# Kernel optimization log

Hardware: AMD Instinct MI355X
Metric: run time of the kernel (lower is better)

Reference implementation:

```python
import jax, jax.numpy as jnp
import numpy as np

N = 50000
V = 3
DIM = 128
H = 64


def setup_inputs() -> dict:
    key = jax.random.key(0)
    ks = jax.random.split(key, 8)
    x = jax.random.normal(ks[0], (N, V * DIM), dtype=jnp.float32)
    edge_index = jax.random.randint(ks[1], (2, 800000), 0, N, dtype=jnp.int64)
    Wv = jax.random.normal(ks[2], (V, DIM, H), dtype=jnp.float32) * (1.0 / np.sqrt(DIM))
    bv = jnp.zeros((V, H), dtype=jnp.float32)
    na_w = jax.random.normal(ks[3], (H, 1), dtype=jnp.float32) * (1.0 / np.sqrt(H))
    na_b = jnp.zeros((1,), dtype=jnp.float32)
    va_w1 = jax.random.normal(ks[4], (H, H // 2), dtype=jnp.float32) * (1.0 / np.sqrt(H))
    va_b1 = jnp.zeros((H // 2,), dtype=jnp.float32)
    va_w2 = jax.random.normal(ks[5], (H // 2, 1), dtype=jnp.float32) * (1.0 / np.sqrt(H // 2))
    va_b2 = jnp.zeros((1,), dtype=jnp.float32)
    cls_w = jax.random.normal(ks[6], (H, 2), dtype=jnp.float32) * (1.0 / np.sqrt(H))
    cls_b = jnp.zeros((2,), dtype=jnp.float32)
    return dict(x=x, edge_index=edge_index, Wv=Wv, bv=bv, na_w=na_w, na_b=na_b,
                va_w1=va_w1, va_b1=va_b1, va_w2=va_w2, va_b2=va_b2,
                cls_w=cls_w, cls_b=cls_b)


def reference(x, edge_index, Wv, bv, na_w, na_b, va_w1, va_b1, va_w2, va_b2, cls_w, cls_b):
    n = x.shape[0]
    # split into equal-dim views: [N, V, DIM]
    xv = x.reshape(n, V, DIM)

    # --- GCNConv (PyG defaults): linear transform, add self-loops, sym-norm aggregate, bias ---
    h = jnp.einsum('nvd,vdh->nvh', xv, Wv)  # [N, V, H]

    src = edge_index[0]
    dst = edge_index[1]
    loop = jnp.arange(n, dtype=src.dtype)
    src_full = jnp.concatenate([src, loop])
    dst_full = jnp.concatenate([dst, loop])

    ones = jnp.ones(src_full.shape[0], dtype=h.dtype)
    deg = jax.ops.segment_sum(ones, dst_full, num_segments=n)  # in-degree incl. self-loop
    dinv = jnp.where(deg > 0, 1.0 / jnp.sqrt(deg), 0.0)
    norm = dinv[src_full] * dinv[dst_full]  # [E+N]

    msgs = h[src_full] * norm[:, None, None]            # [E+N, V, H]
    agg = jax.ops.segment_sum(msgs, dst_full, num_segments=n)  # [N, V, H]
    agg = agg + bv[None, :, :]

    # ReLU
    emb = jax.nn.relu(agg)  # [N, V, H]

    # --- NodeAttentionLayer: softmax over nodes (dim=0), applied per view ---
    scores = jnp.einsum('nvh,ho->nvo', emb, na_w) + na_b  # [N, V, 1]
    att = jax.nn.softmax(scores, axis=0)
    emb_w = emb * att  # [N, V, H]

    # --- ViewAttention ---
    avg = jnp.mean(emb_w, axis=0)  # [V, H]
    vs = jnp.tanh(avg @ va_w1 + va_b1) @ va_w2 + va_b2  # [V, 1]
    vw = jax.nn.softmax(vs.T, axis=1)  # [1, V]
    fused = jnp.einsum('nvh,v->nh', emb_w, vw[0])  # [N, H]

    # --- classifier + log_softmax ---
    logits = fused @ cls_w + cls_b
    logp = jax.nn.log_softmax(logits, axis=1)
    return logp, fused, vw[0]
```

## Files before the change

kernel.cpp:

```cpp
#include <hip/hip_runtime.h>
#include <math.h>

#define NV 3
#define DIMX 128
#define HD 64
#define NVH 192
#define NBLK 256
#define NBUK 128
#define BSH 9

typedef unsigned int uint32;
typedef unsigned short ushort16;
typedef unsigned char uchar;
typedef __attribute__((ext_vector_type(8))) short short8;
typedef __attribute__((ext_vector_type(4))) float f32x4;

__device__ __forceinline__ unsigned fkey(float f){
  unsigned b = __float_as_uint(f);
  return (b & 0x80000000u) ? ~b : (b | 0x80000000u);
}
__device__ __forceinline__ float unkey(unsigned k){
  return __uint_as_float((k & 0x80000000u) ? (k ^ 0x80000000u) : ~k);
}
__device__ __forceinline__ uint32 bf16rne(float f){
  uint32 u = __float_as_uint(f);
  return (u + 0x7fffu + ((u >> 16) & 1u)) >> 16;
}
__device__ __forceinline__ float bfus(uint32 q){ return __uint_as_float(q << 16); }
__device__ __forceinline__ float ub0(uint32 p){ return (float)(p & 0xffu); }
__device__ __forceinline__ float ub1(uint32 p){ return (float)((p >> 8) & 0xffu); }
__device__ __forceinline__ float ub2(uint32 p){ return (float)((p >> 16) & 0xffu); }

__global__ void k_zero(float* __restrict__ wsum, float* __restrict__ sumexp, unsigned* __restrict__ maxkey){
  int t = threadIdx.x;
  if (t < NVH) wsum[t] = 0.f;
  else if (t < NVH+3) sumexp[t-NVH] = 0.f;
  else if (t < NVH+6) maxkey[t-NVH-3] = 0u;
}

__global__ __launch_bounds__(256) void k_hist(const int* __restrict__ ei, int E, int EPB,
                                              int* __restrict__ histT){
  __shared__ int sh[NBUK];
  int t = threadIdx.x, b = blockIdx.x;
  if (t < NBUK) sh[t] = 0;
  __syncthreads();
  int e0 = b*EPB, e1 = min(e0 + EPB, E);
  for (int i = e0 + t; i < e1; i += 256){
    int d = ei[E + i];
    atomicAdd(&sh[d >> BSH], 1);
  }
  __syncthreads();
  if (t < NBUK) histT[t*NBLK + b] = sh[t];
}

__global__ __launch_bounds__(1024) void k_hscan(int* __restrict__ histT){
  __shared__ int sh[1024];
  int t = threadIdx.x;
  int lo = t*32;
  int vals[32]; int s = 0;
  #pragma unroll
  for (int k = 0; k < 32; ++k){ vals[k] = histT[lo+k]; s += vals[k]; }
  sh[t] = s; __syncthreads();
  for (int ofs = 1; ofs < 1024; ofs <<= 1){
    int v = (t >= ofs) ? sh[t-ofs] : 0;
    __syncthreads();
    sh[t] += v;
    __syncthreads();
  }
  int run = sh[t] - s;
  #pragma unroll
  for (int k = 0; k < 32; ++k){ histT[lo+k] = run; run += vals[k]; }
}

__global__ __launch_bounds__(256) void k_scatter(const int* __restrict__ ei, int E, int EPB,
                                                 const int* __restrict__ ofsT, uint32* __restrict__ ebuf){
  __shared__ int cur[NBUK];
  int t = threadIdx.x, b = blockIdx.x;
  if (t < NBUK) cur[t] = ofsT[t*NBLK + b];
  __syncthreads();
  int e0 = b*EPB, e1 = min(e0 + EPB, E);
  for (int i = e0 + t; i < e1; i += 256){
    int s = ei[i], d = ei[E + i];
    int pos = atomicAdd(&cur[d >> BSH], 1);
    ebuf[pos] = ((uint32)(d & 511) << 16) | (uint32)s;
  }
}

__global__ __launch_bounds__(512) void k_csr(const uint32* __restrict__ ebuf, const int* __restrict__ ofsT,
                                             int E, int N, int* __restrict__ rowstart,
                                             float* __restrict__ dinv, int* __restrict__ csr){
  __shared__ int cnt[512];
  __shared__ int pre[512];
  int t = threadIdx.x, b = blockIdx.x;
  int estart = ofsT[b*NBLK];
  int eend   = ((b+1)*NBLK < NBUK*NBLK) ? ofsT[(b+1)*NBLK] : E;
  int n0 = b << BSH;
  int nn = min(512, N - n0);
  cnt[t] = 0;
  __syncthreads();
  for (int i = estart + t; i < eend; i += 512){
    atomicAdd(&cnt[ebuf[i] >> 16], 1);
  }
  __syncthreads();
  int c = cnt[t];
  pre[t] = c;
  __syncthreads();
  for (int ofs = 1; ofs < 512; ofs <<= 1){
    int v = (t >= ofs) ? pre[t-ofs] : 0;
    __syncthreads();
    pre[t] += v;
    __syncthreads();
  }
  int excl = pre[t] - c;
  if (t < nn){
    rowstart[n0 + t] = estart + excl;
    dinv[n0 + t] = rsqrtf((float)(c + 1));
  }
  if (b == gridDim.x - 1 && t == 0) rowstart[N] = E;
  cnt[t] = estart + excl;
  __syncthreads();
  for (int i = estart + t; i < eend; i += 512){
    uint32 e = ebuf[i];
    int pos = atomicAdd(&cnt[e >> 16], 1);
    csr[pos] = (int)(e & 0xFFFFu);
  }
}

__global__ __launch_bounds__(256) void k_wpack(const float* __restrict__ Wv, uint32* __restrict__ Wb){
  int t = blockIdx.x*blockDim.x + threadIdx.x;
  if (t >= 3072) return;
  int l = t & 63, s = (t >> 6) & 3, c = (t >> 8) & 3, v = t >> 10;
  int h = c*16 + (l & 15);
  int kbase = s*32 + (l >> 4)*8;
  const float* wp = Wv + v*8192 + h;
  uint32 o[4];
  #pragma unroll
  for (int jj = 0; jj < 4; ++jj){
    uint32 lo = bf16rne(wp[(kbase + 2*jj    )*64]);
    uint32 hi = bf16rne(wp[(kbase + 2*jj + 1)*64]);
    o[jj] = lo | (hi << 16);
  }
  Wb[t*4+0] = o[0]; Wb[t*4+1] = o[1]; Wb[t*4+2] = o[2]; Wb[t*4+3] = o[3];
}

__global__ __launch_bounds__(256) void k_h(const float* __restrict__ x, const uint32* __restrict__ Wb,
                                           const float* __restrict__ dinv,
                                           uchar* __restrict__ hq8, float* __restrict__ scale4,
                                           int N, int NT){
  int wv = (blockIdx.x*blockDim.x + threadIdx.x) >> 6;
  int lane = threadIdx.x & 63;
  int tile = wv / 3;
  int v = wv - tile*3;
  if (tile >= NT) return;
  int jrow = lane & 15;
  int kq   = lane >> 4;
  int nrow = tile*16 + jrow;
  const float* xr = x + (size_t)nrow*384 + v*128 + kq*8;
  const short8* WB = (const short8*)Wb;

  f32x4 acc[4] = {};
  #pragma unroll
  for (int s = 0; s < 4; ++s){
    const float* p = xr + s*32;
    float4 f = *(const float4*)p, g = *(const float4*)(p+4);
    short8 a;
    a[0]=(short)bf16rne(f.x); a[1]=(short)bf16rne(f.y); a[2]=(short)bf16rne(f.z); a[3]=(short)bf16rne(f.w);
    a[4]=(short)bf16rne(g.x); a[5]=(short)bf16rne(g.y); a[6]=(short)bf16rne(g.z); a[7]=(short)bf16rne(g.w);
    #pragma unroll
    for (int c = 0; c < 4; ++c){
      short8 b = WB[(v*4 + c)*256 + s*64 + lane];
      acc[c] = __builtin_amdgcn_mfma_f32_16x16x32_bf16(a, b, acc[c], 0, 0, 0);
    }
  }

  float vv[4][4];
  float mx = 0.f;
  #pragma unroll
  for (int r = 0; r < 4; ++r){
    int n = tile*16 + kq*4 + r;
    float dv = dinv[n];
    #pragma unroll
    for (int c = 0; c < 4; ++c){
      float t = acc[c][r]*dv;
      vv[c][r] = t;
      mx = fmaxf(mx, fabsf(t));
    }
  }
  #pragma unroll
  for (int ofs = 1; ofs < 64; ofs <<= 1) mx = fmaxf(mx, __shfl_xor(mx, ofs));
  float inv = (mx > 0.f) ? 127.0f/mx : 0.f;
  #pragma unroll
  for (int r = 0; r < 4; ++r){
    int n = tile*16 + kq*4 + r;
    #pragma unroll
    for (int c = 0; c < 4; ++c){
      uint32 q = (uint32)(int)(vv[c][r]*inv + 128.5f);
      hq8[(size_t)n*256 + (c*16 + jrow)*4 + v] = (uchar)q;
    }
  }
  if (lane == 0) scale4[tile*4 + v] = mx * (1.0f/127.0f);
}

__global__ __launch_bounds__(256) void k_aggv(const uint32* __restrict__ hq4, const float4* __restrict__ sc4,
                                              const int* __restrict__ rowstart, const int* __restrict__ csr,
                                              const float* __restrict__ dinv, const float* __restrict__ bv,
                                              const float* __restrict__ na_w, const float* __restrict__ na_b,
                                              ushort16* __restrict__ emb, float* __restrict__ scores, int N){
  int wid = (blockIdx.x*blockDim.x + threadIdx.x) >> 6;
  int lane = threadIdx.x & 63;
  if (wid >= N) return;
  int n = wid;
  uint32 ps = hq4[(size_t)n*64 + lane];
  float4 cs = sc4[n >> 4];
  float a0 = cs.x*ub0(ps), a1 = cs.y*ub1(ps), a2 = cs.z*ub2(ps);
  float ss0 = cs.x, ss1 = cs.y, ss2 = cs.z;
  int r0 = rowstart[n], r1 = rowstart[n+1];
  for (int base = r0; base < r1; base += 64){
    int m = r1 - base; if (m > 64) m = 64;
    int sv = (lane < m) ? __builtin_nontemporal_load(&csr[base + lane]) : 0;
    int i = 0;
    for (; i + 3 < m; i += 4){
      int s0 = __shfl(sv, i), s1 = __shfl(sv, i+1), s2 = __shfl(sv, i+2), s3 = __shfl(sv, i+3);
      uint32 p0 = hq4[(size_t)s0*64 + lane];
      uint32 p1 = hq4[(size_t)s1*64 + lane];
      uint32 p2 = hq4[(size_t)s2*64 + lane];
      uint32 p3 = hq4[(size_t)s3*64 + lane];
      float4 f0 = sc4[s0 >> 4];
      float4 f1 = sc4[s1 >> 4];
      float4 f2 = sc4[s2 >> 4];
      float4 f3 = sc4[s3 >> 4];
      a0 = fmaf(f0.x, ub0(p0), a0); a1 = fmaf(f0.y, ub1(p0), a1); a2 = fmaf(f0.z, ub2(p0), a2);
      a0 = fmaf(f1.x, ub0(p1), a0); a1 = fmaf(f1.y, ub1(p1), a1); a2 = fmaf(f1.z, ub2(p1), a2);
      a0 = fmaf(f2.x, ub0(p2), a0); a1 = fmaf(f2.y, ub1(p2), a1); a2 = fmaf(f2.z, ub2(p2), a2);
      a0 = fmaf(f3.x, ub0(p3), a0); a1 = fmaf(f3.y, ub1(p3), a1); a2 = fmaf(f3.z, ub2(p3), a2);
      ss0 += f0.x + f1.x + f2.x + f3.x;
      ss1 += f0.y + f1.y + f2.y + f3.y;
      ss2 += f0.z + f1.z + f2.z + f3.z;
    }
    for (; i < m; ++i){
      int s = __shfl(sv, i);
      uint32 p = hq4[(size_t)s*64 + lane];
      float4 f = sc4[s >> 4];
      a0 = fmaf(f.x, ub0(p), a0); a1 = fmaf(f.y, ub1(p), a1); a2 = fmaf(f.z, ub2(p), a2);
      ss0 += f.x; ss1 += f.y; ss2 += f.z;
    }
  }
  a0 -= 128.0f*ss0;
  a1 -= 128.0f*ss1;
  a2 -= 128.0f*ss2;
  float dv = dinv[n];
  float e0 = fmaxf(a0*dv + bv[lane],      0.f);
  float e1 = fmaxf(a1*dv + bv[64+lane],   0.f);
  float e2 = fmaxf(a2*dv + bv[128+lane],  0.f);
  ushort16* ep = emb + (size_t)n*NVH;
  __builtin_nontemporal_store((ushort16)bf16rne(e0), &ep[lane]);
  __builtin_nontemporal_store((ushort16)bf16rne(e1), &ep[64+lane]);
  __builtin_nontemporal_store((ushort16)bf16rne(e2), &ep[128+lane]);
  float w = na_w[lane];
  float s0 = e0*w, s1 = e1*w, s2 = e2*w;
  #pragma unroll
  for (int ofs = 32; ofs >= 1; ofs >>= 1){
    s0 += __shfl_xor(s0, ofs);
    s1 += __shfl_xor(s1, ofs);
    s2 += __shfl_xor(s2, ofs);
  }
  if (lane == 0){
    float nb = na_b[0];
    scores[n] = s0 + nb; scores[N + n] = s1 + nb; scores[2*N + n] = s2 + nb;
  }
}

__global__ void k_max(const float* __restrict__ scores, int N, unsigned* __restrict__ maxkey){
  __shared__ float sh[256];
  int v = blockIdx.y;
  const float* sp = scores + (size_t)v*N;
  int base = blockIdx.x*2048 + threadIdx.x;
  float m = -3.0e38f;
  #pragma unroll
  for (int k = 0; k < 8; ++k){
    int i = base + k*256;
    if (i < N) m = fmaxf(m, sp[i]);
  }
  sh[threadIdx.x] = m; __syncthreads();
  for (int ofs = 128; ofs >= 1; ofs >>= 1){
    if (threadIdx.x < ofs) sh[threadIdx.x] = fmaxf(sh[threadIdx.x], sh[threadIdx.x+ofs]);
    __syncthreads();
  }
  if (threadIdx.x == 0) atomicMax(&maxkey[v], fkey(sh[0]));
}

__global__ __launch_bounds__(256) void k_wsum(const ushort16* __restrict__ emb, const float* __restrict__ scores,
                                              const unsigned* __restrict__ maxkey, float* __restrict__ wsum,
                                              float* __restrict__ sumexp, int N){
  __shared__ float shw[4][NVH];
  __shared__ float shse[4][4];
  int t = threadIdx.x;
  int lane = t & 63;
  int wv = t >> 6;
  int gw = (blockIdx.x*blockDim.x + t) >> 6;
  int nw = (gridDim.x*blockDim.x) >> 6;
  float m0 = unkey(maxkey[0]), m1 = unkey(maxkey[1]), m2 = unkey(maxkey[2]);
  float w0=0.f, w1=0.f, w2=0.f, se0=0.f, se1=0.f, se2=0.f;
  for (int n = gw; n < N; n += nw){
    const ushort16* ep = emb + (size_t)n*NVH;
    float x0 = expf(scores[n]       - m0);
    float x1 = expf(scores[N + n]   - m1);
    float x2 = expf(scores[2*N + n] - m2);
    w0 += bfus(ep[lane])*x0; w1 += bfus(ep[64+lane])*x1; w2 += bfus(ep[128+lane])*x2;
    se0 += x0; se1 += x1; se2 += x2;
  }
  shw[wv][lane]     = w0;
  shw[wv][64+lane]  = w1;
  shw[wv][128+lane] = w2;
  #pragma unroll
  for (int ofs = 32; ofs >= 1; ofs >>= 1){
    se0 += __shfl_xor(se0, ofs);
    se1 += __shfl_xor(se1, ofs);
    se2 += __shfl_xor(se2, ofs);
  }
  if (lane == 0){ shse[wv][0] = se0; shse[wv][1] = se1; shse[wv][2] = se2; }
  __syncthreads();
  if (t < NVH){
    float s = shw[0][t] + shw[1][t] + shw[2][t] + shw[3][t];
    atomicAdd(&wsum[t], s);
  } else if (t >= NVH && t < NVH+3){
    int v = t - NVH;
    float s = shse[0][v] + shse[1][v] + shse[2][v] + shse[3][v];
    atomicAdd(&sumexp[v], s);
  }
}

__global__ __launch_bounds__(64) void k_view(const float* __restrict__ wsum, const float* __restrict__ sumexp,
                                             const float* __restrict__ va_w1, const float* __restrict__ va_b1,
                                             const float* __restrict__ va_w2, const float* __restrict__ va_b2,
                                             float* __restrict__ g, float* __restrict__ out_vw, int N){
  __shared__ float avg[NV][64];
  __shared__ float z1[NV][32];
  int t = threadIdx.x;
  if (t < 64){
    for (int v = 0; v < NV; ++v) avg[v][t] = wsum[v*64+t] / (sumexp[v] * (float)N);
  }
  __syncthreads();
  if (t < 32){
    for (int v = 0; v < NV; ++v){
      float a = va_b1[t];
      for (int h = 0; h < 64; ++h) a += avg[v][h]*va_w1[h*32 + t];
      z1[v][t] = tanhf(a);
    }
  }
  __syncthreads();
  if (t == 0){
    float vs[NV];
    for (int v = 0; v < NV; ++v){
      float a = va_b2[0];
      for (int j = 0; j < 32; ++j) a += z1[v][j]*va_w2[j];
      vs[v] = a;
    }
    float m = fmaxf(vs[0], fmaxf(vs[1], vs[2]));
    float e0 = expf(vs[0]-m), e1 = expf(vs[1]-m), e2 = expf(vs[2]-m);
    float inv = 1.f/(e0+e1+e2);
    float vw0 = e0*inv, vw1 = e1*inv, vw2 = e2*inv;
    out_vw[0] = vw0; out_vw[1] = vw1; out_vw[2] = vw2;
    g[0] = vw0/sumexp[0]; g[1] = vw1/sumexp[1]; g[2] = vw2/sumexp[2];
  }
}

__global__ __launch_bounds__(256) void k_fused(const ushort16* __restrict__ emb, const float* __restrict__ scores,
                                               const unsigned* __restrict__ maxkey, const float* __restrict__ g,
                                               const float* __restrict__ cls_w, const float* __restrict__ cls_b,
                                               float* __restrict__ out, int N){
  int wid = (blockIdx.x*blockDim.x + threadIdx.x) >> 6;
  int lane = threadIdx.x & 63;
  if (wid >= N) return;
  int n = wid;
  float m0 = unkey(maxkey[0]), m1 = unkey(maxkey[1]), m2 = unkey(maxkey[2]);
  float w0 = expf(scores[n]       - m0)*g[0];
  float w1 = expf(scores[N + n]   - m1)*g[1];
  float w2 = expf(scores[2*N + n] - m2)*g[2];
  const ushort16* ep = emb + (size_t)n*NVH;
  float fu = bfus(ep[lane])*w0 + bfus(ep[64+lane])*w1 + bfus(ep[128+lane])*w2;
  out[(size_t)2*N + (size_t)n*64 + lane] = fu;
  float c0 = fu*cls_w[lane*2 + 0];
  float c1 = fu*cls_w[lane*2 + 1];
  #pragma unroll
  for (int ofs = 32; ofs >= 1; ofs >>= 1){
    c0 += __shfl_xor(c0, ofs);
    c1 += __shfl_xor(c1, ofs);
  }
  if (lane == 0){
    float l0 = c0 + cls_b[0], l1 = c1 + cls_b[1];
    float m = fmaxf(l0, l1);
    float lse = m + logf(expf(l0-m) + expf(l1-m));
    out[(size_t)n*2]     = l0 - lse;
    out[(size_t)n*2 + 1] = l1 - lse;
  }
}

extern "C" void kernel_launch(void* const* d_in, const int* in_sizes, int n_in,
                              void* d_out, int out_size, void* d_ws, size_t ws_size,
                              hipStream_t stream){
  const float* x     = (const float*)d_in[0];
  const int*   ei    = (const int*)d_in[1];
  const float* Wv    = (const float*)d_in[2];
  const float* bv    = (const float*)d_in[3];
  const float* na_w  = (const float*)d_in[4];
  const float* na_b  = (const float*)d_in[5];
  const float* va_w1 = (const float*)d_in[6];
  const float* va_b1 = (const float*)d_in[7];
  const float* va_w2 = (const float*)d_in[8];
  const float* va_b2 = (const float*)d_in[9];
  const float* cls_w = (const float*)d_in[10];
  const float* cls_b = (const float*)d_in[11];
  int N = in_sizes[0] / (NV*DIMX);
  int E = in_sizes[1] / 2;
  float* out = (float*)d_out;
  int NT = (N + 15) / 16;

  char* wptr = (char*)d_ws;
  size_t off = 0;
  auto alloc = [&](size_t bytes){ void* p = wptr + off; off += (bytes + 255) & ~255ull; return p; };
  uchar*     hq       = (uchar*)alloc((size_t)N*256);
  float*     scale4   = (float*)alloc((size_t)NT*4*4);
  ushort16*  emb      = (ushort16*)alloc((size_t)N*NVH*2);
  int*       csr      = (int*)alloc((size_t)E*4);
  uint32*    ebuf     = (uint32*)alloc((size_t)E*4);
  int*       histT    = (int*)alloc((size_t)NBUK*NBLK*4);
  int*       rowstart = (int*)alloc((size_t)(N+1)*4);
  float*     dinv     = (float*)alloc((size_t)N*4);
  float*     scores   = (float*)alloc((size_t)3*N*4);
  unsigned*  maxkey   = (unsigned*)alloc(3*4);
  float*     sumexp   = (float*)alloc(3*4);
  float*     wsum     = (float*)alloc(192*4);
  float*     g        = (float*)alloc(3*4);
  uint32*    Wb       = (uint32*)alloc(3072*16);

  int EPB = (E + NBLK - 1) / NBLK;
  int nbuck = (N + 511) >> BSH;
  k_zero   <<<1, 256, 0, stream>>>(wsum, sumexp, maxkey);
  k_hist   <<<NBLK, 256, 0, stream>>>(ei, E, EPB, histT);
  k_hscan  <<<1, 1024, 0, stream>>>(histT);
  k_scatter<<<NBLK, 256, 0, stream>>>(ei, E, EPB, histT, ebuf);
  k_csr    <<<nbuck, 512, 0, stream>>>(ebuf, histT, E, N, rowstart, dinv, csr);
  k_wpack  <<<12, 256, 0, stream>>>(Wv, Wb);
  int hwaves = NT*3;
  k_h      <<<(hwaves*64+255)/256, 256, 0, stream>>>(x, Wb, dinv, hq, scale4, N, NT);
  k_aggv   <<<(N*64+255)/256, 256, 0, stream>>>((const uint32*)hq, (const float4*)scale4, rowstart, csr,
                                                dinv, bv, na_w, na_b, emb, scores, N);
  dim3 gm((N+2047)/2048, NV);
  k_max    <<<gm, 256, 0, stream>>>(scores, N, maxkey);
  k_wsum   <<<304, 256, 0, stream>>>(emb, scores, maxkey, wsum, sumexp, N);
  k_view   <<<1, 64, 0, stream>>>(wsum, sumexp, va_w1, va_b1, va_w2, va_b2, g,
                                  out + (size_t)2*N + (size_t)N*64, N);
  k_fused  <<<(N*64+255)/256, 256, 0, stream>>>(emb, scores, maxkey, g, cls_w, cls_b, out, N);
}
```

Measured before the change: 164.5 us.

## Compact int8 hidden layout to 192 bytes per node and pack bf16 embeddings

The quantized hidden rows are stored densely at 192 bytes per node instead of padded 4-byte slots at 256 bytes. In k_aggv each of 48 lanes now gathers one dword holding four features of a single view, cutting the bytes moved per neighbor gather. Embeddings are written as packed bf16 pairs, and k_wsum and k_fused are rewritten for the new layout. The k_zero launch is folded into k_wpack. The price is 16 idle lanes per wave in the aggregation kernel, plus a k_wsum that carries a leftover dead loop and a redundant extra pass over view 2.

```diff
diff --git a/kernel.cpp b/kernel.cpp
--- a/kernel.cpp
+++ b/kernel.cpp
@@ -14,6 +14,7 @@
 typedef unsigned char uchar;
 typedef __attribute__((ext_vector_type(8))) short short8;
 typedef __attribute__((ext_vector_type(4))) float f32x4;
+typedef __attribute__((ext_vector_type(2))) unsigned int u32x2;
 
 __device__ __forceinline__ unsigned fkey(float f){
   unsigned b = __float_as_uint(f);
@@ -30,13 +31,7 @@
 __device__ __forceinline__ float ub0(uint32 p){ return (float)(p & 0xffu); }
 __device__ __forceinline__ float ub1(uint32 p){ return (float)((p >> 8) & 0xffu); }
 __device__ __forceinline__ float ub2(uint32 p){ return (float)((p >> 16) & 0xffu); }
-
-__global__ void k_zero(float* __restrict__ wsum, float* __restrict__ sumexp, unsigned* __restrict__ maxkey){
-  int t = threadIdx.x;
-  if (t < NVH) wsum[t] = 0.f;
-  else if (t < NVH+3) sumexp[t-NVH] = 0.f;
-  else if (t < NVH+6) maxkey[t-NVH-3] = 0u;
-}
+__device__ __forceinline__ float ub3(uint32 p){ return (float)(p >> 24); }
 
 __global__ __launch_bounds__(256) void k_hist(const int* __restrict__ ei, int E, int EPB,
                                               int* __restrict__ histT){
@@ -126,8 +121,16 @@
   }
 }
 
-__global__ __launch_bounds__(256) void k_wpack(const float* __restrict__ Wv, uint32* __restrict__ Wb){
+__global__ __launch_bounds__(256) void k_wpack(const float* __restrict__ Wv, uint32* __restrict__ Wb,
+                                               float* __restrict__ wsum, float* __restrict__ sumexp,
+                                               unsigned* __restrict__ maxkey){
   int t = blockIdx.x*blockDim.x + threadIdx.x;
+  if (blockIdx.x == 0){
+    int u = threadIdx.x;
+    if (u < NVH) wsum[u] = 0.f;
+    else if (u < NVH+3) sumexp[u-NVH] = 0.f;
+    else if (u < NVH+6) maxkey[u-NVH-3] = 0u;
+  }
   if (t >= 3072) return;
   int l = t & 63, s = (t >> 6) & 3, c = (t >> 8) & 3, v = t >> 10;
   int h = c*16 + (l & 15);
@@ -195,25 +198,27 @@
     #pragma unroll
     for (int c = 0; c < 4; ++c){
       uint32 q = (uint32)(int)(vv[c][r]*inv + 128.5f);
-      hq8[(size_t)n*256 + (c*16 + jrow)*4 + v] = (uchar)q;
+      hq8[(size_t)n*192 + v*64 + c*16 + jrow] = (uchar)q;
     }
   }
   if (lane == 0) scale4[tile*4 + v] = mx * (1.0f/127.0f);
 }
 
-__global__ __launch_bounds__(256) void k_aggv(const uint32* __restrict__ hq4, const float4* __restrict__ sc4,
+__global__ __launch_bounds__(256) void k_aggv(const uint32* __restrict__ hq4, const float* __restrict__ sc,
                                               const int* __restrict__ rowstart, const int* __restrict__ csr,
                                               const float* __restrict__ dinv, const float* __restrict__ bv,
                                               const float* __restrict__ na_w, const float* __restrict__ na_b,
-                                              ushort16* __restrict__ emb, float* __restrict__ scores, int N){
+                                              uint32* __restrict__ emb, float* __restrict__ scores, int N){
   int wid = (blockIdx.x*blockDim.x + threadIdx.x) >> 6;
   int lane = threadIdx.x & 63;
   if (wid >= N) return;
   int n = wid;
-  uint32 ps = hq4[(size_t)n*64 + lane];
-  float4 cs = sc4[n >> 4];
-  float a0 = cs.x*ub0(ps), a1 = cs.y*ub1(ps), a2 = cs.z*ub2(ps);
-  float ss0 = cs.x, ss1 = cs.y, ss2 = cs.z;
+  int jl = (lane < 48) ? lane : 0;
+  int v = jl >> 4;
+  uint32 ps = hq4[(size_t)n*48 + jl];
+  float cs = sc[((n >> 4) << 2) + v];
+  float a0 = cs*ub0(ps), a1 = cs*ub1(ps), a2 = cs*ub2(ps), a3 = cs*ub3(ps);
+  float ssum = cs;
   int r0 = rowstart[n], r1 = rowstart[n+1];
   for (int base = r0; base < r1; base += 64){
     int m = r1 - base; if (m > 64) m = 64;
@@ -221,53 +226,49 @@
     int i = 0;
     for (; i + 3 < m; i += 4){
       int s0 = __shfl(sv, i), s1 = __shfl(sv, i+1), s2 = __shfl(sv, i+2), s3 = __shfl(sv, i+3);
-      uint32 p0 = hq4[(size_t)s0*64 + lane];
-      uint32 p1 = hq4[(size_t)s1*64 + lane];
-      uint32 p2 = hq4[(size_t)s2*64 + lane];
-      uint32 p3 = hq4[(size_t)s3*64 + lane];
-      float4 f0 = sc4[s0 >> 4];
-      float4 f1 = sc4[s1 >> 4];
-      float4 f2 = sc4[s2 >> 4];
-      float4 f3 = sc4[s3 >> 4];
-      a0 = fmaf(f0.x, ub0(p0), a0); a1 = fmaf(f0.y, ub1(p0), a1); a2 = fmaf(f0.z, ub2(p0), a2);
-      a0 = fmaf(f1.x, ub0(p1), a0); a1 = fmaf(f1.y, ub1(p1), a1); a2 = fmaf(f1.z, ub2(p1), a2);
-      a0 = fmaf(f2.x, ub0(p2), a0); a1 = fmaf(f2.y, ub1(p2), a1); a2 = fmaf(f2.z, ub2(p2), a2);
-      a0 = fmaf(f3.x, ub0(p3), a0); a1 = fmaf(f3.y, ub1(p3), a1); a2 = fmaf(f3.z, ub2(p3), a2);
-      ss0 += f0.x + f1.x + f2.x + f3.x;
-      ss1 += f0.y + f1.y + f2.y + f3.y;
-      ss2 += f0.z + f1.z + f2.z + f3.z;
+      uint32 p0 = hq4[(size_t)s0*48 + jl];
+      uint32 p1 = hq4[(size_t)s1*48 + jl];
+      uint32 p2 = hq4[(size_t)s2*48 + jl];
+      uint32 p3 = hq4[(size_t)s3*48 + jl];
+      float f0 = sc[((s0 >> 4) << 2) + v];
+      float f1 = sc[((s1 >> 4) << 2) + v];
+      float f2 = sc[((s2 >> 4) << 2) + v];
+      float f3 = sc[((s3 >> 4) << 2) + v];
+      a0 = fmaf(f0, ub0(p0), a0); a1 = fmaf(f0, ub1(p0), a1); a2 = fmaf(f0, ub2(p0), a2); a3 = fmaf(f0, ub3(p0), a3);
+      a0 = fmaf(f1, ub0(p1), a0); a1 = fmaf(f1, ub1(p1), a1); a2 = fmaf(f1, ub2(p1), a2); a3 = fmaf(f1, ub3(p1), a3);
+      a0 = fmaf(f2, ub0(p2), a0); a1 = fmaf(f2, ub1(p2), a1); a2 = fmaf(f2, ub2(p2), a2); a3 = fmaf(f2, ub3(p2), a3);
+      a0 = fmaf(f3, ub0(p3), a0); a1 = fmaf(f3, ub1(p3), a1); a2 = fmaf(f3, ub2(p3), a2); a3 = fmaf(f3, ub3(p3), a3);
+      ssum += f0 + f1 + f2 + f3;
     }
     for (; i < m; ++i){
       int s = __shfl(sv, i);
-      uint32 p = hq4[(size_t)s*64 + lane];
-      float4 f = sc4[s >> 4];
-      a0 = fmaf(f.x, ub0(p), a0); a1 = fmaf(f.y, ub1(p), a1); a2 = fmaf(f.z, ub2(p), a2);
-      ss0 += f.x; ss1 += f.y; ss2 += f.z;
-    }
-  }
-  a0 -= 128.0f*ss0;
-  a1 -= 128.0f*ss1;
-  a2 -= 128.0f*ss2;
+      uint32 p = hq4[(size_t)s*48 + jl];
+      float f = sc[((s >> 4) << 2) + v];
+      a0 = fmaf(f, ub0(p), a0); a1 = fmaf(f, ub1(p), a1); a2 = fmaf(f, ub2(p), a2); a3 = fmaf(f, ub3(p), a3);
+      ssum += f;
+    }
+  }
+  float off128 = 128.0f*ssum;
+  a0 -= off128; a1 -= off128; a2 -= off128; a3 -= off128;
   float dv = dinv[n];
-  float e0 = fmaxf(a0*dv + bv[lane],      0.f);
-  float e1 = fmaxf(a1*dv + bv[64+lane],   0.f);
-  float e2 = fmaxf(a2*dv + bv[128+lane],  0.f);
-  ushort16* ep = emb + (size_t)n*NVH;
-  __builtin_nontemporal_store((ushort16)bf16rne(e0), &ep[lane]);
-  __builtin_nontemporal_store((ushort16)bf16rne(e1), &ep[64+lane]);
-  __builtin_nontemporal_store((ushort16)bf16rne(e2), &ep[128+lane]);
-  float w = na_w[lane];
-  float s0 = e0*w, s1 = e1*w, s2 = e2*w;
-  #pragma unroll
-  for (int ofs = 32; ofs >= 1; ofs >>= 1){
-    s0 += __shfl_xor(s0, ofs);
-    s1 += __shfl_xor(s1, ofs);
-    s2 += __shfl_xor(s2, ofs);
-  }
-  if (lane == 0){
-    float nb = na_b[0];
-    scores[n] = s0 + nb; scores[N + n] = s1 + nb; scores[2*N + n] = s2 + nb;
-  }
+  float4 bb = *(const float4*)&bv[jl*4];
+  float e0 = fmaxf(a0*dv + bb.x, 0.f);
+  float e1 = fmaxf(a1*dv + bb.y, 0.f);
+  float e2 = fmaxf(a2*dv + bb.z, 0.f);
+  float e3 = fmaxf(a3*dv + bb.w, 0.f);
+  if (lane < 48){
+    u32x2 pk;
+    pk.x = bf16rne(e0) | (bf16rne(e1) << 16);
+    pk.y = bf16rne(e2) | (bf16rne(e3) << 16);
+    __builtin_nontemporal_store(pk, (u32x2*)(emb + (size_t)n*96 + 2*jl));
+  }
+  float4 nw = *(const float4*)&na_w[(jl & 15)*4];
+  float s = e0*nw.x + e1*nw.y + e2*nw.z + e3*nw.w;
+  s += __shfl_xor(s, 1);
+  s += __shfl_xor(s, 2);
+  s += __shfl_xor(s, 4);
+  s += __shfl_xor(s, 8);
+  if (lane < 48 && (lane & 15) == 0) scores[(size_t)v*N + n] = s + na_b[0];
 }
 
 __global__ void k_max(const float* __restrict__ scores, int N, unsigned* __restrict__ maxkey){
@@ -289,7 +290,7 @@
   if (threadIdx.x == 0) atomicMax(&maxkey[v], fkey(sh[0]));
 }
 
-__global__ __launch_bounds__(256) void k_wsum(const ushort16* __restrict__ emb, const float* __restrict__ scores,
+__global__ __launch_bounds__(256) void k_wsum(const uint32* __restrict__ emb, const float* __restrict__ scores,
                                               const unsigned* __restrict__ maxkey, float* __restrict__ wsum,
                                               float* __restrict__ sumexp, int N){
   __shared__ float shw[4][NVH];
@@ -302,16 +303,61 @@
   float m0 = unkey(maxkey[0]), m1 = unkey(maxkey[1]), m2 = unkey(maxkey[2]);
   float w0=0.f, w1=0.f, w2=0.f, se0=0.f, se1=0.f, se2=0.f;
   for (int n = gw; n < N; n += nw){
-    const ushort16* ep = emb + (size_t)n*NVH;
+    const uint32* ep = emb + (size_t)n*96;
+    uint32 pa = ep[lane];
+    uint32 pb = ep[64+lane];
     float x0 = expf(scores[n]       - m0);
     float x1 = expf(scores[N + n]   - m1);
     float x2 = expf(scores[2*N + n] - m2);
-    w0 += bfus(ep[lane])*x0; w1 += bfus(ep[64+lane])*x1; w2 += bfus(ep[128+lane])*x2;
+    int f0v = (2*lane) >> 6;
+    int f1v = (128 + 2*lane) >> 6;
+    float xa = (f0v == 0) ? x0 : x1;
+    float xb = x2;
+    w0 += (bfus(pa & 0xffffu) + 0.f)*xa;
+    (void)pb; (void)xb; (void)w1; (void)w2;
+    break;
+  }
+  w0 = w1 = w2 = 0.f; se0 = se1 = se2 = 0.f;
+  for (int n = gw; n < N; n += nw){
+    const uint32* ep = emb + (size_t)n*96;
+    float x0 = expf(scores[n]       - m0);
+    float x1 = expf(scores[N + n]   - m1);
+    float x2 = expf(scores[2*N + n] - m2);
+    uint32 pa = ep[lane];
+    uint32 pb = ep[32+lane];
+    (void)pb;
+    int fd = 2*lane;
+    float xlo = (fd < 64) ? x0 : (fd < 128) ? x1 : x2;
+    int fd1 = fd + 1;
+    float xhi = (fd1 < 64) ? x0 : (fd1 < 128) ? x1 : x2;
+    w0 += bfus(pa & 0xffffu)*xlo;
+    w1 += bfus(pa >> 16)*xhi;
+    uint32 pc = ep[64+lane];
+    int fe = 128 + 2*lane;
+    float ylo = (fe < 128) ? x1 : x2;
+    float yhi = ylo;
+    w2 += bfus(pc & 0xffffu)*ylo + bfus(pc >> 16)*yhi;
     se0 += x0; se1 += x1; se2 += x2;
   }
-  shw[wv][lane]     = w0;
-  shw[wv][64+lane]  = w1;
-  shw[wv][128+lane] = w2;
+  __shared__ float acc[NVH];
+  if (t < NVH) acc[t] = 0.f;
+  __syncthreads();
+  float w2lo = 0.f, w2hi = 0.f;
+  for (int n = gw; n < N; n += nw){
+    const uint32* ep = emb + (size_t)n*96;
+    float x2 = expf(scores[2*N + n] - m2);
+    uint32 pc = ep[64+lane];
+    w2lo += bfus(pc & 0xffffu)*x2;
+    w2hi += bfus(pc >> 16)*x2;
+  }
+  atomicAdd(&acc[2*lane],       w0);
+  atomicAdd(&acc[2*lane+1],     w1);
+  if (lane < 32){
+    atomicAdd(&acc[128+2*lane],   w2lo);
+    atomicAdd(&acc[128+2*lane+1], w2hi);
+  }
+  __syncthreads();
+  if (t < NVH) atomicAdd(&wsum[t], acc[t]);
   #pragma unroll
   for (int ofs = 32; ofs >= 1; ofs >>= 1){
     se0 += __shfl_xor(se0, ofs);
@@ -320,14 +366,11 @@
   }
   if (lane == 0){ shse[wv][0] = se0; shse[wv][1] = se1; shse[wv][2] = se2; }
   __syncthreads();
-  if (t < NVH){
-    float s = shw[0][t] + shw[1][t] + shw[2][t] + shw[3][t];
-    atomicAdd(&wsum[t], s);
-  } else if (t >= NVH && t < NVH+3){
-    int v = t - NVH;
-    float s = shse[0][v] + shse[1][v] + shse[2][v] + shse[3][v];
-    atomicAdd(&sumexp[v], s);
-  }
+  if (t < 3){
+    float s = shse[0][t] + shse[1][t] + shse[2][t] + shse[3][t];
+    atomicAdd(&sumexp[t], s);
+  }
+  (void)shw;
 }
 
 __global__ __launch_bounds__(64) void k_view(const float* __restrict__ wsum, const float* __restrict__ sumexp,
@@ -365,7 +408,7 @@
   }
 }
 
-__global__ __launch_bounds__(256) void k_fused(const ushort16* __restrict__ emb, const float* __restrict__ scores,
+__global__ __launch_bounds__(256) void k_fused(const uint32* __restrict__ emb, const float* __restrict__ scores,
                                                const unsigned* __restrict__ maxkey, const float* __restrict__ g,
                                                const float* __restrict__ cls_w, const float* __restrict__ cls_b,
                                                float* __restrict__ out, int N){
@@ -377,8 +420,15 @@
   float w0 = expf(scores[n]       - m0)*g[0];
   float w1 = expf(scores[N + n]   - m1)*g[1];
   float w2 = expf(scores[2*N + n] - m2)*g[2];
-  const ushort16* ep = emb + (size_t)n*NVH;
-  float fu = bfus(ep[lane])*w0 + bfus(ep[64+lane])*w1 + bfus(ep[128+lane])*w2;
+  const uint32* ep = emb + (size_t)n*96;
+  int dw = lane >> 1, hi = lane & 1;
+  uint32 p0 = ep[dw];
+  uint32 p1 = ep[32 + dw];
+  uint32 p2 = ep[64 + dw];
+  float v0 = hi ? bfus(p0 >> 16) : bfus(p0 & 0xffffu);
+  float v1 = hi ? bfus(p1 >> 16) : bfus(p1 & 0xffffu);
+  float v2 = hi ? bfus(p2 >> 16) : bfus(p2 & 0xffffu);
+  float fu = v0*w0 + v1*w1 + v2*w2;
   out[(size_t)2*N + (size_t)n*64 + lane] = fu;
   float c0 = fu*cls_w[lane*2 + 0];
   float c1 = fu*cls_w[lane*2 + 1];
@@ -419,9 +469,9 @@
   char* wptr = (char*)d_ws;
   size_t off = 0;
   auto alloc = [&](size_t bytes){ void* p = wptr + off; off += (bytes + 255) & ~255ull; return p; };
-  uchar*     hq       = (uchar*)alloc((size_t)N*256);
+  uchar*     hq       = (uchar*)alloc((size_t)N*192);
   float*     scale4   = (float*)alloc((size_t)NT*4*4);
-  ushort16*  emb      = (ushort16*)alloc((size_t)N*NVH*2);
+  uint32*    emb      = (uint32*)alloc((size_t)N*96*4);
   int*       csr      = (int*)alloc((size_t)E*4);
   uint32*    ebuf     = (uint32*)alloc((size_t)E*4);
   int*       histT    = (int*)alloc((size_t)NBUK*NBLK*4);
@@ -436,15 +486,14 @@
 
   int EPB = (E + NBLK - 1) / NBLK;
   int nbuck = (N + 511) >> BSH;
-  k_zero   <<<1, 256, 0, stream>>>(wsum, sumexp, maxkey);
   k_hist   <<<NBLK, 256, 0, stream>>>(ei, E, EPB, histT);
   k_hscan  <<<1, 1024, 0, stream>>>(histT);
   k_scatter<<<NBLK, 256, 0, stream>>>(ei, E, EPB, histT, ebuf);
   k_csr    <<<nbuck, 512, 0, stream>>>(ebuf, histT, E, N, rowstart, dinv, csr);
-  k_wpack  <<<12, 256, 0, stream>>>(Wv, Wb);
+  k_wpack  <<<12, 256, 0, stream>>>(Wv, Wb, wsum, sumexp, maxkey);
   int hwaves = NT*3;
   k_h      <<<(hwaves*64+255)/256, 256, 0, stream>>>(x, Wb, dinv, hq, scale4, N, NT);
-  k_aggv   <<<(N*64+255)/256, 256, 0, stream>>>((const uint32*)hq, (const float4*)scale4, rowstart, csr,
+  k_aggv   <<<(N*64+255)/256, 256, 0, stream>>>((const uint32*)hq, scale4, rowstart, csr,
                                                 dinv, bv, na_w, na_b, emb, scores, N);
   dim3 gm((N+2047)/2048, NV);
   k_max    <<<gm, 256, 0, stream>>>(scores, N, maxkey);
```

After: 169.5 us. 1.03x slower.
